# Optimization experiments

Measured on AMD Instinct MI355X. Metric: run time of the kernel, lower is better.

## Reference

```python
import jax, jax.numpy as jnp
import numpy as np

SUPPORT = 8
NEIGH = 32
EPS = 1e-6


def setup_inputs() -> dict:
    key = jax.random.key(0)
    xyz = jax.random.normal(key, (4, 4096, 3), dtype=jnp.float32)
    return {"xyz": xyz}


def _gather(points, idx):
    # points: (B, N, D), idx: (B, N, K) -> (B, N, K, D)
    return jax.vmap(lambda p, i: p[i])(points, idx)


def _forward(xyz):
    B, N, _ = xyz.shape
    # brute-force squared pairwise distances (B, N, N)
    sq = jnp.sum(xyz * xyz, axis=-1)
    d = sq[:, :, None] + sq[:, None, :] - 2.0 * jnp.einsum('bnd,bmd->bnm', xyz, xyz)
    # k nearest neighbors, ascending distance; idx[...,0] is the point itself
    _, idx = jax.lax.top_k(-d, NEIGH)  # (B, N, NEIGH)

    # --- PCA normal estimation (pytorch3d estimate_pointcloud_normals) ---
    nbrs = _gather(xyz, idx)                      # (B, N, K, 3)
    ctr = nbrs.mean(axis=2, keepdims=True)
    X = nbrs - ctr
    cov = jnp.einsum('bnki,bnkj->bnij', X, X)     # (B, N, 3, 3)
    _, v = jnp.linalg.eigh(cov)                   # eigenvalues ascending
    normals = v[..., :, 0]                        # eigenvector of smallest eigenvalue
    # disambiguate direction: flip so normal agrees with offsets to neighbors
    df = nbrs - xyz[:, :, None, :]                # (B, N, K, 3)
    proj = jnp.einsum('bnd,bnkd->bnk', normals, df).sum(-1)
    normals = jnp.where((proj < 0.0)[..., None], -normals, normals)  # (B, N, 3)

    # --- KNN (support) gather of normals; same metric, sorted, so slice ---
    idx_s = idx[..., :SUPPORT]                    # (B, N, S)
    nn_normals = _gather(normals, idx_s)          # (B, N, S, 3)

    # cosine similarity between self normal and each neighbor normal
    anchor = nn_normals[:, :, 0:1, :]             # (B, N, 1, 3)
    na = jnp.maximum(jnp.linalg.norm(anchor, axis=-1), EPS)
    nb = jnp.maximum(jnp.linalg.norm(nn_normals, axis=-1), EPS)
    cos = jnp.sum(anchor * nn_normals, axis=-1) / (na * nb)  # (B, N, S)

    penalty = 1.0 - cos
    penalty = penalty.std(axis=-1, ddof=1)        # torch .std default unbiased
    return penalty.mean(axis=-1)                  # (B,)


def reference(xyz):
    return _forward(xyz)
```

## Files before the change

kernel.cpp:

```cpp
#include <hip/hip_runtime.h>

typedef unsigned int uint;

#define NPTS 4096
#define BLK  256
#define KNN  32
#define KSUP 8
#define NBIN 1024
#define MAXC 352
#define LINSCALE 16.0f

__global__ __launch_bounds__(256) void pack_kernel(
        const float* __restrict__ xyz, float4* __restrict__ pts4, int total)
{
    int i = blockIdx.x * BLK + threadIdx.x;
    if (i < total) {
        float x = xyz[i*3+0], y = xyz[i*3+1], z = xyz[i*3+2];
        pts4[i] = make_float4(x, y, z, x*x + y*y + z*z);
    }
}

__device__ __forceinline__ uint fkey(float d) {
    uint u = __float_as_uint(d);
    return u ^ ((u & 0x80000000u) ? 0xFFFFFFFFu : 0x80000000u);
}
__device__ __forceinline__ uint linbin(float d) {
    return (uint)fmaxf(fminf(d * LINSCALE, 1023.0f), 0.0f);
}

__device__ __forceinline__ void find_cross(const uint* hist, uint* s_bin, int tid) {
    if (tid < 64) {
        const uint4* h4 = (const uint4*)hist;
        uint4 h0 = h4[tid*4+0], h1 = h4[tid*4+1], h2 = h4[tid*4+2], h3 = h4[tid*4+3];
        uint s = h0.x+h0.y+h0.z+h0.w + h1.x+h1.y+h1.z+h1.w
               + h2.x+h2.y+h2.z+h2.w + h3.x+h3.y+h3.z+h3.w;
        uint t = s;
        #pragma unroll
        for (int off = 1; off < 64; off <<= 1) {
            uint u = __shfl_up(t, off, 64);
            if (tid >= off) t += u;
        }
        uint ex = t - s;
        if (ex < KNN && ex + s >= KNN) {
            uint cum = ex, binoff = 0;
            cum += h0.x; binoff += (cum < KNN); cum += h0.y; binoff += (cum < KNN);
            cum += h0.z; binoff += (cum < KNN); cum += h0.w; binoff += (cum < KNN);
            cum += h1.x; binoff += (cum < KNN); cum += h1.y; binoff += (cum < KNN);
            cum += h1.z; binoff += (cum < KNN); cum += h1.w; binoff += (cum < KNN);
            cum += h2.x; binoff += (cum < KNN); cum += h2.y; binoff += (cum < KNN);
            cum += h2.z; binoff += (cum < KNN); cum += h2.w; binoff += (cum < KNN);
            cum += h3.x; binoff += (cum < KNN); cum += h3.y; binoff += (cum < KNN);
            cum += h3.z; binoff += (cum < KNN); cum += h3.w; binoff += (cum < KNN);
            *s_bin = tid * 16u + binoff;
        }
    }
}

__global__ __launch_bounds__(256) void knn_cov_kernel(
        const float4* __restrict__ pts4,
        float* __restrict__ covS,
        int*   __restrict__ idx8)
{
    const int pid = blockIdx.x;
    const int b   = pid >> 12;
    const int n   = pid & (NPTS - 1);
    const int tid = threadIdx.x;
    const float4* P = pts4 + (size_t)b * NPTS;

    __shared__ uint hist[NBIN];
    __shared__ uint s_bin;
    __shared__ uint s_mode;
    __shared__ uint coll_cnt;
    __shared__ uint ckey[MAXC];
    __shared__ int  cidx[MAXC];
    __shared__ int  sel[KNN];

    const float4 q = P[n];
    const float qx = q.x, qy = q.y, qz = q.z, sqn = q.w;

    const float t0 = 0.1606f * __expf(sqn * (1.0f / 3.0f));

    if (tid == 0) { coll_cnt = 0; s_mode = 0; }
    __syncthreads();

    #pragma unroll 4
    for (int m = tid; m < NPTS; m += BLK) {
        float4 p = P[m];
        float d = sqn + p.w - 2.0f * (qx * p.x + qy * p.y + qz * p.z);
        if (d < t0) {
            uint pos = atomicAdd(&coll_cnt, 1u);
            if (pos < MAXC) { ckey[pos] = fkey(d); cidx[pos] = m; }
        }
    }
    __syncthreads();

    uint cnt = coll_cnt;
    if (cnt < KNN || cnt > MAXC) {
        if (tid == 0) { s_mode = 1; coll_cnt = 0; }
        #pragma unroll
        for (int i = 0; i < NBIN / BLK; ++i) hist[tid + i * BLK] = 0;
        __syncthreads();

        #pragma unroll 4
        for (int m = tid; m < NPTS; m += BLK) {
            float4 p = P[m];
            float d = sqn + p.w - 2.0f * (qx * p.x + qy * p.y + qz * p.z);
            atomicAdd(&hist[linbin(d)], 1u);
        }
        __syncthreads();
        find_cross(hist, &s_bin, tid);
        __syncthreads();
        uint lin_ok = (s_bin != 1023u);
        if (!lin_ok) {
            #pragma unroll
            for (int i = 0; i < NBIN / BLK; ++i) hist[tid + i * BLK] = 0;
            __syncthreads();
            for (int m = tid; m < NPTS; m += BLK) {
                float4 p = P[m];
                float d = sqn + p.w - 2.0f * (qx * p.x + qy * p.y + qz * p.z);
                atomicAdd(&hist[fkey(d) >> 22], 1u);
            }
            __syncthreads();
            find_cross(hist, &s_bin, tid);
            __syncthreads();
        }
        const uint bmax = s_bin;
        for (int m = tid; m < NPTS; m += BLK) {
            float4 p = P[m];
            float d = sqn + p.w - 2.0f * (qx * p.x + qy * p.y + qz * p.z);
            uint k = fkey(d);
            uint bin = lin_ok ? linbin(d) : (k >> 22);
            if (bin <= bmax) {
                uint pos = atomicAdd(&coll_cnt, 1u);
                if (pos < MAXC) { ckey[pos] = k; cidx[pos] = m; }
            }
        }
        __syncthreads();
    }
    const int M = (int)min(coll_cnt, (uint)MAXC);

    for (int i = tid; i < M; i += BLK) {
        uint uk = ckey[i]; int ui = cidx[i];
        int r = 0;
        for (int j = 0; j < M; ++j) {
            uint vk = ckey[j];
            r += (vk < uk || (vk == uk && cidx[j] < ui)) ? 1 : 0;
        }
        if (r < KNN) sel[r] = ui;
    }
    __syncthreads();

    if (tid < 32) {
        int j = sel[tid];
        float4 pj = P[j];
        float q0 = pj.x, q1 = pj.y, q2 = pj.z;

        float s0 = q0, s1 = q1, s2 = q2;
        #pragma unroll
        for (int ml = 1; ml < 32; ml <<= 1) {
            s0 += __shfl_xor(s0, ml, 32);
            s1 += __shfl_xor(s1, ml, 32);
            s2 += __shfl_xor(s2, ml, 32);
        }
        const float c0 = s0 * (1.0f/32.0f), c1 = s1 * (1.0f/32.0f), c2 = s2 * (1.0f/32.0f);
        const float X0 = q0 - c0, X1 = q1 - c1, X2 = q2 - c2;
        float xx = X0*X0, xy = X0*X1, xz = X0*X2, yy = X1*X1, yz = X1*X2, zz = X2*X2;
        #pragma unroll
        for (int ml = 1; ml < 32; ml <<= 1) {
            xx += __shfl_xor(xx, ml, 32);
            xy += __shfl_xor(xy, ml, 32);
            xz += __shfl_xor(xz, ml, 32);
            yy += __shfl_xor(yy, ml, 32);
            yz += __shfl_xor(yz, ml, 32);
            zz += __shfl_xor(zz, ml, 32);
        }
        if (tid == 0) {
            float4* o = (float4*)(covS + (size_t)pid * 12);
            o[0] = make_float4(xx, xy, xz, yy);
            o[1] = make_float4(yz, zz, s0 - 32.0f*qx, s1 - 32.0f*qy);
            o[2] = make_float4(s2 - 32.0f*qz, 0.0f, 0.0f, 0.0f);
        }
    }
    if (tid < KSUP) idx8[(size_t)pid*KSUP + tid] = sel[tid];
}

__global__ __launch_bounds__(256) void eig_kernel(
        const float* __restrict__ covS, float* __restrict__ normals, int total)
{
    const int pid = blockIdx.x * BLK + threadIdx.x;
    if (pid >= total) return;
    const float4* c4 = (const float4*)(covS + (size_t)pid * 12);
    const float4 a = c4[0], bb = c4[1], cc = c4[2];

    double A00 = a.x, A01 = a.y, A02 = a.z, A11 = a.w, A12 = bb.x, A22 = bb.y;
    const float S0 = bb.z, S1 = bb.w, S2 = cc.x;
    double V00=1, V01=0, V02=0, V10=0, V11=1, V12=0, V20=0, V21=0, V22=1;

    #pragma unroll
    for (int sweep = 0; sweep < 5; ++sweep) {
        {
            double apq = A01;
            if (fabs(apq) > 1e-300) {
                double th = (A11 - A00) / (2.0*apq);
                double t  = (th >= 0.0 ? 1.0 : -1.0) / (fabs(th) + sqrt(th*th + 1.0));
                double c  = 1.0/sqrt(t*t + 1.0), s = t*c;
                double a00 = c*c*A00 - 2.0*s*c*A01 + s*s*A11;
                double a11 = s*s*A00 + 2.0*s*c*A01 + c*c*A11;
                double a02 = c*A02 - s*A12;
                double a12 = s*A02 + c*A12;
                A00 = a00; A11 = a11; A01 = 0.0; A02 = a02; A12 = a12;
                double v0, v1;
                v0 = V00; v1 = V01; V00 = c*v0 - s*v1; V01 = s*v0 + c*v1;
                v0 = V10; v1 = V11; V10 = c*v0 - s*v1; V11 = s*v0 + c*v1;
                v0 = V20; v1 = V21; V20 = c*v0 - s*v1; V21 = s*v0 + c*v1;
            }
        }
        {
            double apq = A02;
            if (fabs(apq) > 1e-300) {
                double th = (A22 - A00) / (2.0*apq);
                double t  = (th >= 0.0 ? 1.0 : -1.0) / (fabs(th) + sqrt(th*th + 1.0));
                double c  = 1.0/sqrt(t*t + 1.0), s = t*c;
                double a00 = c*c*A00 - 2.0*s*c*A02 + s*s*A22;
                double a22 = s*s*A00 + 2.0*s*c*A02 + c*c*A22;
                double a01 = c*A01 - s*A12;
                double a12 = s*A01 + c*A12;
                A00 = a00; A22 = a22; A02 = 0.0; A01 = a01; A12 = a12;
                double v0, v1;
                v0 = V00; v1 = V02; V00 = c*v0 - s*v1; V02 = s*v0 + c*v1;
                v0 = V10; v1 = V12; V10 = c*v0 - s*v1; V12 = s*v0 + c*v1;
                v0 = V20; v1 = V22; V20 = c*v0 - s*v1; V22 = s*v0 + c*v1;
            }
        }
        {
            double apq = A12;
            if (fabs(apq) > 1e-300) {
                double th = (A22 - A11) / (2.0*apq);
                double t  = (th >= 0.0 ? 1.0 : -1.0) / (fabs(th) + sqrt(th*th + 1.0));
                double c  = 1.0/sqrt(t*t + 1.0), s = t*c;
                double a11 = c*c*A11 - 2.0*s*c*A12 + s*s*A22;
                double a22 = s*s*A11 + 2.0*s*c*A12 + c*c*A22;
                double a01 = c*A01 - s*A02;
                double a02 = s*A01 + c*A02;
                A11 = a11; A22 = a22; A12 = 0.0; A01 = a01; A02 = a02;
                double v0, v1;
                v0 = V01; v1 = V02; V01 = c*v0 - s*v1; V02 = s*v0 + c*v1;
                v0 = V11; v1 = V12; V11 = c*v0 - s*v1; V12 = s*v0 + c*v1;
                v0 = V21; v1 = V22; V21 = c*v0 - s*v1; V22 = s*v0 + c*v1;
            }
        }
    }

    double e0 = A00, e1 = A11, e2 = A22;
    double v0, v1, v2;
    if (e0 <= e1 && e0 <= e2)      { v0 = V00; v1 = V10; v2 = V20; }
    else if (e1 <= e0 && e1 <= e2) { v0 = V01; v1 = V11; v2 = V21; }
    else                           { v0 = V02; v1 = V12; v2 = V22; }
    double nrm = sqrt(v0*v0 + v1*v1 + v2*v2);
    if (nrm > 0.0) { v0 /= nrm; v1 /= nrm; v2 /= nrm; }

    float f0 = (float)v0, f1 = (float)v1, f2 = (float)v2;
    float proj = f0*S0 + f1*S1 + f2*S2;
    if (proj < 0.0f) { f0 = -f0; f1 = -f1; f2 = -f2; }
    normals[(size_t)pid*3+0] = f0;
    normals[(size_t)pid*3+1] = f1;
    normals[(size_t)pid*3+2] = f2;
}

__global__ __launch_bounds__(256) void penalty_kernel(
        const float* __restrict__ normals,
        const int*   __restrict__ idx8,
        float*       __restrict__ out)
{
    const int pid = blockIdx.x * BLK + threadIdx.x;
    const int b   = pid >> 12;
    const int* my = idx8 + (size_t)pid * KSUP;
    const float* nb_base = normals + (size_t)b * NPTS * 3;

    const int i0 = my[0];
    const float a0 = nb_base[i0*3+0], a1 = nb_base[i0*3+1], a2 = nb_base[i0*3+2];
    const float na = fmaxf(sqrtf(a0*a0 + a1*a1 + a2*a2), 1e-6f);

    float p[KSUP];
    float sum = 0.0f;
    #pragma unroll
    for (int k = 0; k < KSUP; ++k) {
        int ik = my[k];
        float b0 = nb_base[ik*3+0], b1 = nb_base[ik*3+1], b2 = nb_base[ik*3+2];
        float nbn = fmaxf(sqrtf(b0*b0 + b1*b1 + b2*b2), 1e-6f);
        float cosv = (a0*b0 + a1*b1 + a2*b2) / (na * nbn);
        p[k] = 1.0f - cosv;
        sum += p[k];
    }
    const float mean = sum * (1.0f / 8.0f);
    float var = 0.0f;
    #pragma unroll
    for (int k = 0; k < KSUP; ++k) { float dv = p[k] - mean; var += dv * dv; }
    float v = sqrtf(var * (1.0f / 7.0f)) * (1.0f / 4096.0f);

    #pragma unroll
    for (int ml = 1; ml < 64; ml <<= 1) v += __shfl_xor(v, ml, 64);
    __shared__ float red[4];
    if ((threadIdx.x & 63) == 0) red[threadIdx.x >> 6] = v;
    __syncthreads();
    if (threadIdx.x == 0) {
        atomicAdd(&out[b], red[0] + red[1] + red[2] + red[3]);
    }
}

extern "C" void kernel_launch(void* const* d_in, const int* in_sizes, int n_in,
                              void* d_out, int out_size, void* d_ws, size_t ws_size,
                              hipStream_t stream) {
    const float* xyz = (const float*)d_in[0];
    float* out = (float*)d_out;

    const int B = in_sizes[0] / (NPTS * 3);
    const int total = B * NPTS;

    char* ws = (char*)d_ws;
    float4* pts4   = (float4*)ws;                       ws += (size_t)total * sizeof(float4);
    float*  covS   = (float*)ws;                        ws += (size_t)total * 12 * sizeof(float);
    float*  normals= (float*)ws;                        ws += (size_t)total * 3 * sizeof(float);
    int*    idx8   = (int*)ws;

    hipMemsetAsync(d_out, 0, (size_t)out_size * sizeof(float), stream);

    hipLaunchKernelGGL(pack_kernel, dim3((total + BLK - 1) / BLK), dim3(BLK), 0, stream,
                       xyz, pts4, total);
    hipLaunchKernelGGL(knn_cov_kernel, dim3(total), dim3(BLK), 0, stream,
                       pts4, covS, idx8);
    hipLaunchKernelGGL(eig_kernel, dim3((total + BLK - 1) / BLK), dim3(BLK), 0, stream,
                       covS, normals, total);
    hipLaunchKernelGGL(penalty_kernel, dim3(total / BLK), dim3(BLK), 0, stream,
                       normals, idx8, out);
}
```

Before: 154.6 us.

## Process eight queries per block with shared-memory point tiles in KNN

The KNN kernel now handles eight query points per block, 32 threads each, and stages point tiles in shared memory so all queries reuse each loaded tile. The old design had one block per query and reread all points from global memory each time. Queries whose threshold candidate count misses the bounds fall back to a serialized block-wide histogram path, with an exact O(N^2) rank as the last resort. The smaller kernels also switch to 64-thread blocks, and the penalty reduction drops its shared-memory step.

```diff
diff --git a/kernel.cpp b/kernel.cpp
--- a/kernel.cpp
+++ b/kernel.cpp
@@ -4,16 +4,21 @@
 
 #define NPTS 4096
 #define BLK  256
+#define QPB  8
+#define TPQ  32
 #define KNN  32
 #define KSUP 8
+#define TILE 512
+#define NTILE (NPTS/TILE)
+#define MAXCQ 192
+#define FBCAP (QPB*MAXCQ)
 #define NBIN 1024
-#define MAXC 352
 #define LINSCALE 16.0f
 
-__global__ __launch_bounds__(256) void pack_kernel(
+__global__ __launch_bounds__(64) void pack_kernel(
         const float* __restrict__ xyz, float4* __restrict__ pts4, int total)
 {
-    int i = blockIdx.x * BLK + threadIdx.x;
+    int i = blockIdx.x * 64 + threadIdx.x;
     if (i < total) {
         float x = xyz[i*3+0], y = xyz[i*3+1], z = xyz[i*3+2];
         pts4[i] = make_float4(x, y, z, x*x + y*y + z*z);
@@ -61,101 +66,140 @@
         float* __restrict__ covS,
         int*   __restrict__ idx8)
 {
-    const int pid = blockIdx.x;
-    const int b   = pid >> 12;
-    const int n   = pid & (NPTS - 1);
+    const int bid = blockIdx.x;
+    const int b   = bid / (NPTS / QPB);
+    const int qg  = bid % (NPTS / QPB);
     const int tid = threadIdx.x;
+    const int g   = tid >> 5;
+    const int t   = tid & 31;
+    const int n   = qg * QPB + g;
+    const int pid = b * NPTS + n;
     const float4* P = pts4 + (size_t)b * NPTS;
 
-    __shared__ uint hist[NBIN];
-    __shared__ uint s_bin;
-    __shared__ uint s_mode;
-    __shared__ uint coll_cnt;
-    __shared__ uint ckey[MAXC];
-    __shared__ int  cidx[MAXC];
-    __shared__ int  sel[KNN];
+    __shared__ float4 stage[TILE];
+    __shared__ uint ckey[QPB][MAXCQ];
+    __shared__ int  cidx[QPB][MAXCQ];
+    __shared__ int  sel[QPB][KNN];
+    __shared__ uint ccnt[QPB];
+    __shared__ uint s_flag;
+    __shared__ uint s_bin, s_cnt2;
 
     const float4 q = P[n];
     const float qx = q.x, qy = q.y, qz = q.z, sqn = q.w;
-
     const float t0 = 0.1606f * __expf(sqn * (1.0f / 3.0f));
 
-    if (tid == 0) { coll_cnt = 0; s_mode = 0; }
+    if (tid < QPB) ccnt[tid] = 0;
+    if (tid == 0) s_flag = 0;
     __syncthreads();
 
-    #pragma unroll 4
-    for (int m = tid; m < NPTS; m += BLK) {
-        float4 p = P[m];
-        float d = sqn + p.w - 2.0f * (qx * p.x + qy * p.y + qz * p.z);
-        if (d < t0) {
-            uint pos = atomicAdd(&coll_cnt, 1u);
-            if (pos < MAXC) { ckey[pos] = fkey(d); cidx[pos] = m; }
-        }
+    for (int tile = 0; tile < NTILE; ++tile) {
+        const int base = tile * TILE;
+        stage[tid]       = P[base + tid];
+        stage[tid + BLK] = P[base + tid + BLK];
+        __syncthreads();
+        #pragma unroll 4
+        for (int k = 0; k < TILE / TPQ; ++k) {
+            const int j = t + k * TPQ;
+            float4 p = stage[j];
+            float d = sqn + p.w - 2.0f * (qx * p.x + qy * p.y + qz * p.z);
+            if (d < t0) {
+                uint pos = atomicAdd(&ccnt[g], 1u);
+                if (pos < MAXCQ) { ckey[g][pos] = fkey(d); cidx[g][pos] = base + j; }
+            }
+        }
+        __syncthreads();
+    }
+
+    if (t == 0) {
+        uint c = ccnt[g];
+        if (c < KNN || c > MAXCQ) atomicOr(&s_flag, 1u << g);
     }
     __syncthreads();
-
-    uint cnt = coll_cnt;
-    if (cnt < KNN || cnt > MAXC) {
-        if (tid == 0) { s_mode = 1; coll_cnt = 0; }
-        #pragma unroll
-        for (int i = 0; i < NBIN / BLK; ++i) hist[tid + i * BLK] = 0;
-        __syncthreads();
-
-        #pragma unroll 4
-        for (int m = tid; m < NPTS; m += BLK) {
-            float4 p = P[m];
-            float d = sqn + p.w - 2.0f * (qx * p.x + qy * p.y + qz * p.z);
-            atomicAdd(&hist[linbin(d)], 1u);
-        }
-        __syncthreads();
-        find_cross(hist, &s_bin, tid);
-        __syncthreads();
-        uint lin_ok = (s_bin != 1023u);
-        if (!lin_ok) {
-            #pragma unroll
-            for (int i = 0; i < NBIN / BLK; ++i) hist[tid + i * BLK] = 0;
+    const uint flags = s_flag;
+
+    if (!((flags >> g) & 1u)) {
+        const int M = (int)ccnt[g];
+        for (int i = t; i < M; i += TPQ) {
+            uint uk = ckey[g][i]; int ui = cidx[g][i];
+            int r = 0;
+            for (int j = 0; j < M; ++j) {
+                uint vk = ckey[g][j];
+                r += (vk < uk || (vk == uk && cidx[g][j] < ui)) ? 1 : 0;
+            }
+            if (r < KNN) sel[g][r] = ui;
+        }
+    }
+    __syncthreads();
+
+    if (flags) {
+        uint* hist   = (uint*)stage;
+        uint* fkeys  = &ckey[0][0];
+        int*  fidx   = &cidx[0][0];
+        for (int g2 = 0; g2 < QPB; ++g2) {
+            if (!((flags >> g2) & 1u)) continue;
+            const int n2 = qg * QPB + g2;
+            const float4 q2 = P[n2];
+            const float q2x = q2.x, q2y = q2.y, q2z = q2.z, sq2 = q2.w;
+
+            for (int i = tid; i < NBIN; i += BLK) hist[i] = 0;
+            if (tid == 0) s_cnt2 = 0;
             __syncthreads();
             for (int m = tid; m < NPTS; m += BLK) {
                 float4 p = P[m];
-                float d = sqn + p.w - 2.0f * (qx * p.x + qy * p.y + qz * p.z);
-                atomicAdd(&hist[fkey(d) >> 22], 1u);
+                float d = sq2 + p.w - 2.0f * (q2x * p.x + q2y * p.y + q2z * p.z);
+                atomicAdd(&hist[linbin(d)], 1u);
             }
             __syncthreads();
             find_cross(hist, &s_bin, tid);
             __syncthreads();
-        }
-        const uint bmax = s_bin;
-        for (int m = tid; m < NPTS; m += BLK) {
-            float4 p = P[m];
-            float d = sqn + p.w - 2.0f * (qx * p.x + qy * p.y + qz * p.z);
-            uint k = fkey(d);
-            uint bin = lin_ok ? linbin(d) : (k >> 22);
-            if (bin <= bmax) {
-                uint pos = atomicAdd(&coll_cnt, 1u);
-                if (pos < MAXC) { ckey[pos] = k; cidx[pos] = m; }
-            }
-        }
-        __syncthreads();
-    }
-    const int M = (int)min(coll_cnt, (uint)MAXC);
-
-    for (int i = tid; i < M; i += BLK) {
-        uint uk = ckey[i]; int ui = cidx[i];
-        int r = 0;
-        for (int j = 0; j < M; ++j) {
-            uint vk = ckey[j];
-            r += (vk < uk || (vk == uk && cidx[j] < ui)) ? 1 : 0;
-        }
-        if (r < KNN) sel[r] = ui;
+            const uint bmax = s_bin;
+            for (int m = tid; m < NPTS; m += BLK) {
+                float4 p = P[m];
+                float d = sq2 + p.w - 2.0f * (q2x * p.x + q2y * p.y + q2z * p.z);
+                if (linbin(d) <= bmax) {
+                    uint pos = atomicAdd(&s_cnt2, 1u);
+                    if (pos < FBCAP) { fkeys[pos] = fkey(d); fidx[pos] = m; }
+                }
+            }
+            __syncthreads();
+            const uint cnt2 = s_cnt2;
+            if (cnt2 <= FBCAP) {
+                const int M2 = (int)cnt2;
+                for (int i = tid; i < M2; i += BLK) {
+                    uint uk = fkeys[i]; int ui = fidx[i];
+                    int r = 0;
+                    for (int j = 0; j < M2; ++j) {
+                        uint vk = fkeys[j];
+                        r += (vk < uk || (vk == uk && fidx[j] < ui)) ? 1 : 0;
+                    }
+                    if (r < KNN) sel[g2][r] = ui;
+                }
+            } else {
+                for (int m = tid; m < NPTS; m += BLK) {
+                    float4 pm = P[m];
+                    float dm = sq2 + pm.w - 2.0f * (q2x * pm.x + q2y * pm.y + q2z * pm.z);
+                    uint km = fkey(dm);
+                    int r = 0;
+                    for (int j = 0; j < NPTS; ++j) {
+                        float4 pj = P[j];
+                        float dj = sq2 + pj.w - 2.0f * (q2x * pj.x + q2y * pj.y + q2z * pj.z);
+                        uint kj = fkey(dj);
+                        r += (kj < km || (kj == km && j < m)) ? 1 : 0;
+                    }
+                    if (r < KNN) sel[g2][r] = m;
+                }
+            }
+            __syncthreads();
+        }
     }
     __syncthreads();
 
-    if (tid < 32) {
-        int j = sel[tid];
-        float4 pj = P[j];
-        float q0 = pj.x, q1 = pj.y, q2 = pj.z;
-
-        float s0 = q0, s1 = q1, s2 = q2;
+    {
+        int jn = sel[g][t];
+        float4 pj = P[jn];
+        float p0 = pj.x, p1 = pj.y, p2 = pj.z;
+
+        float s0 = p0, s1 = p1, s2 = p2;
         #pragma unroll
         for (int ml = 1; ml < 32; ml <<= 1) {
             s0 += __shfl_xor(s0, ml, 32);
@@ -163,7 +207,7 @@
             s2 += __shfl_xor(s2, ml, 32);
         }
         const float c0 = s0 * (1.0f/32.0f), c1 = s1 * (1.0f/32.0f), c2 = s2 * (1.0f/32.0f);
-        const float X0 = q0 - c0, X1 = q1 - c1, X2 = q2 - c2;
+        const float X0 = p0 - c0, X1 = p1 - c1, X2 = p2 - c2;
         float xx = X0*X0, xy = X0*X1, xz = X0*X2, yy = X1*X1, yz = X1*X2, zz = X2*X2;
         #pragma unroll
         for (int ml = 1; ml < 32; ml <<= 1) {
@@ -174,20 +218,20 @@
             yz += __shfl_xor(yz, ml, 32);
             zz += __shfl_xor(zz, ml, 32);
         }
-        if (tid == 0) {
+        if (t == 0) {
             float4* o = (float4*)(covS + (size_t)pid * 12);
             o[0] = make_float4(xx, xy, xz, yy);
             o[1] = make_float4(yz, zz, s0 - 32.0f*qx, s1 - 32.0f*qy);
             o[2] = make_float4(s2 - 32.0f*qz, 0.0f, 0.0f, 0.0f);
         }
-    }
-    if (tid < KSUP) idx8[(size_t)pid*KSUP + tid] = sel[tid];
-}
-
-__global__ __launch_bounds__(256) void eig_kernel(
+        if (t < KSUP) idx8[(size_t)pid*KSUP + t] = sel[g][t];
+    }
+}
+
+__global__ __launch_bounds__(64) void eig_kernel(
         const float* __restrict__ covS, float* __restrict__ normals, int total)
 {
-    const int pid = blockIdx.x * BLK + threadIdx.x;
+    const int pid = blockIdx.x * 64 + threadIdx.x;
     if (pid >= total) return;
     const float4* c4 = (const float4*)(covS + (size_t)pid * 12);
     const float4 a = c4[0], bb = c4[1], cc = c4[2];
@@ -267,12 +311,12 @@
     normals[(size_t)pid*3+2] = f2;
 }
 
-__global__ __launch_bounds__(256) void penalty_kernel(
+__global__ __launch_bounds__(64) void penalty_kernel(
         const float* __restrict__ normals,
         const int*   __restrict__ idx8,
         float*       __restrict__ out)
 {
-    const int pid = blockIdx.x * BLK + threadIdx.x;
+    const int pid = blockIdx.x * 64 + threadIdx.x;
     const int b   = pid >> 12;
     const int* my = idx8 + (size_t)pid * KSUP;
     const float* nb_base = normals + (size_t)b * NPTS * 3;
@@ -300,12 +344,7 @@
 
     #pragma unroll
     for (int ml = 1; ml < 64; ml <<= 1) v += __shfl_xor(v, ml, 64);
-    __shared__ float red[4];
-    if ((threadIdx.x & 63) == 0) red[threadIdx.x >> 6] = v;
-    __syncthreads();
-    if (threadIdx.x == 0) {
-        atomicAdd(&out[b], red[0] + red[1] + red[2] + red[3]);
-    }
+    if (threadIdx.x == 0) atomicAdd(&out[b], v);
 }
 
 extern "C" void kernel_launch(void* const* d_in, const int* in_sizes, int n_in,
@@ -325,12 +364,12 @@
 
     hipMemsetAsync(d_out, 0, (size_t)out_size * sizeof(float), stream);
 
-    hipLaunchKernelGGL(pack_kernel, dim3((total + BLK - 1) / BLK), dim3(BLK), 0, stream,
+    hipLaunchKernelGGL(pack_kernel, dim3((total + 63) / 64), dim3(64), 0, stream,
                        xyz, pts4, total);
-    hipLaunchKernelGGL(knn_cov_kernel, dim3(total), dim3(BLK), 0, stream,
+    hipLaunchKernelGGL(knn_cov_kernel, dim3(total / QPB), dim3(BLK), 0, stream,
                        pts4, covS, idx8);
-    hipLaunchKernelGGL(eig_kernel, dim3((total + BLK - 1) / BLK), dim3(BLK), 0, stream,
+    hipLaunchKernelGGL(eig_kernel, dim3((total + 63) / 64), dim3(64), 0, stream,
                        covS, normals, total);
-    hipLaunchKernelGGL(penalty_kernel, dim3(total / BLK), dim3(BLK), 0, stream,
+    hipLaunchKernelGGL(penalty_kernel, dim3(total / 64), dim3(64), 0, stream,
                        normals, idx8, out);
 }
```

Result: slower. 223.2 us (+44.3%).
